# Optimization experiments

Hardware: AMD Instinct MI355X
Metric: run time of the kernel (lower is better)

Reference implementation:

```python
import jax, jax.numpy as jnp
import numpy as np

D_MODEL = 768
N_HEAD = 12
D_K = D_MODEL // N_HEAD
B, S = 2, 2048


def setup_inputs() -> dict:
    key = jax.random.key(0)
    ks = jax.random.split(key, 13)
    scale = 1.0 / np.sqrt(D_MODEL)
    inp = {
        'q': jax.random.normal(ks[0], (B, S, D_MODEL), jnp.float32),
        'k': jax.random.normal(ks[1], (B, S, D_MODEL), jnp.float32),
        'v': jax.random.normal(ks[2], (B, S, D_MODEL), jnp.float32),
        'Wq': jax.random.normal(ks[3], (D_MODEL, D_MODEL), jnp.float32) * scale,
        'bq': jnp.zeros((D_MODEL,), jnp.float32),
        'Wk': jax.random.normal(ks[4], (D_MODEL, D_MODEL), jnp.float32) * scale,
        'bk': jnp.zeros((D_MODEL,), jnp.float32),
        'Wv': jax.random.normal(ks[5], (D_MODEL, D_MODEL), jnp.float32) * scale,
        'bv': jnp.zeros((D_MODEL,), jnp.float32),
        'Wo': jax.random.normal(ks[6], (D_MODEL, D_MODEL), jnp.float32) * scale,
        'bo': jnp.zeros((D_MODEL,), jnp.float32),
        'mask': jax.random.randint(ks[7], (B, 1, S), 0, 2, jnp.int32),
    }
    return inp


def reference(q, k, v, Wq, bq, Wk, bk, Wv, bv, Wo, bo, mask):
    # project and split heads: [B,S,D] -> [B,H,S,Dk]
    def heads(x, W, b):
        y = x @ W + b
        return y.reshape(B, S, N_HEAD, D_K).transpose(0, 2, 1, 3)

    qh = heads(q, Wq, bq)
    kh = heads(k, Wk, bk)
    vh = heads(v, Wv, bv)
    # full score matrix [B,H,S,S] (intentionally materialized, as in source)
    scores = jnp.einsum('bhqd,bhkd->bhqk', qh, kh) / jnp.sqrt(jnp.float32(D_K))
    m = mask[:, None, :, :]  # [B,1,1,S] broadcast over heads and queries
    scores = jnp.where(m == 0, jnp.float32(-1e9), scores)
    p_attn = jax.nn.softmax(scores, axis=-1)
    # dropout omitted (eval / deterministic reference)
    x = jnp.einsum('bhqk,bhkd->bhqd', p_attn, vh)
    x = x.transpose(0, 2, 1, 3).reshape(B, S, D_MODEL)
    return x @ Wo + bo
```

## Files before the change

kernel.cpp:

```cpp
#include <hip/hip_runtime.h>


#define H_ 12
#define DK_ 64
#define B_DIM 2
#define SEQ 2048
#define DM 768
#define MROWS 4096
#define PER_IN ((size_t)MROWS * DM)
#define QSCALE 0.18033688011112042f

typedef short bf16x8 __attribute__((ext_vector_type(8)));
typedef short bf16x4 __attribute__((ext_vector_type(4)));
typedef float f32x4 __attribute__((ext_vector_type(4)));
typedef float f32x16 __attribute__((ext_vector_type(16)));

__device__ inline unsigned short f2bf(float f) {
    union { float f; unsigned int i; } x; x.f = f;
    unsigned int r = x.i + 0x7fff + ((x.i >> 16) & 1);
    return (unsigned short)(r >> 16);
}

__device__ inline unsigned pack2bf(float lo, float hi) {
#if __has_builtin(__builtin_amdgcn_cvt_pk_bf16_f32)
    auto v = __builtin_amdgcn_cvt_pk_bf16_f32(lo, hi);
    return __builtin_bit_cast(unsigned, v);
#else
    return (unsigned)f2bf(lo) | ((unsigned)f2bf(hi) << 16);
#endif
}

__device__ inline float exp2fast(float x) {
#if __has_builtin(__builtin_amdgcn_exp2f)
    return __builtin_amdgcn_exp2f(x);
#else
    return exp2f(x);
#endif
}

__device__ inline f32x16 mfma32x8(bf16x4 a, bf16x4 b, f32x16 c) {
#if __has_builtin(__builtin_amdgcn_mfma_f32_32x32x8bf16_1k)
    return __builtin_amdgcn_mfma_f32_32x32x8bf16_1k(a, b, c, 0, 0, 0);
#else
    asm("v_mfma_f32_32x32x8_bf16 %0, %1, %2, %0" : "+v"(c) : "v"(a), "v"(b));
    return c;
#endif
}

__device__ inline void gload_lds16(const unsigned short* g, unsigned short* ldsbase,
                                   int lane) {
#if __has_builtin(__builtin_amdgcn_global_load_lds)
    __builtin_amdgcn_global_load_lds(
        (const __attribute__((address_space(1))) unsigned int*)g,
        (__attribute__((address_space(3))) unsigned int*)ldsbase, 16, 0, 0);
#else
    *(uint4*)(ldsbase + 8 * lane) = *(const uint4*)g;
#endif
}

__global__ __launch_bounds__(256) void prep(
    const float* __restrict__ q, const float* __restrict__ k,
    const float* __restrict__ v,
    unsigned short* __restrict__ qb, unsigned short* __restrict__ kb,
    unsigned short* __restrict__ vb,
    const float* __restrict__ w0, const float* __restrict__ w1,
    const float* __restrict__ w2, const float* __restrict__ w3,
    unsigned short* __restrict__ wtbase,
    const int* __restrict__ mask, int* __restrict__ idx,
    int* __restrict__ nkeys) {
    __shared__ unsigned short t[32][33];
    __shared__ int wsum[4];
    int job = blockIdx.x, tid = threadIdx.x;
    if (job < 9216) {
        int buf = job / 3072, x = job % 3072;
        const float* src = buf == 0 ? q : (buf == 1 ? k : v);
        unsigned short* dst = buf == 0 ? qb : (buf == 1 ? kb : vb);
        size_t i = ((size_t)x * 256 + tid) * 4;
        float4 f = *(const float4*)(src + i);
        ushort4 u;
        u.x = f2bf(f.x); u.y = f2bf(f.y); u.z = f2bf(f.z); u.w = f2bf(f.w);
        *(ushort4*)(dst + i) = u;
    } else if (job < 11520) {
        int tb = job - 9216;
        int z = tb / 576, r = tb % 576, by = r / 24, bx = r % 24;
        const float* in = z == 0 ? w0 : (z == 1 ? w1 : (z == 2 ? w2 : w3));
        unsigned short* out = wtbase + (size_t)z * DM * DM;
        int x = tid & 31, y = tid >> 5;
        int k0 = bx * 32, n0 = by * 32;
#pragma unroll
        for (int i = 0; i < 32; i += 8)
            t[y + i][x] = f2bf(in[(size_t)(k0 + y + i) * DM + n0 + x]);
        __syncthreads();
#pragma unroll
        for (int i = 0; i < 32; i += 8)
            out[(size_t)(n0 + y + i) * DM + k0 + x] = t[x][y + i];
    } else {
        int b = job - 11520;
        int lane = tid & 63, wave = tid >> 6;
        const int* mp = mask + (size_t)b * SEQ + tid * 8;
        int4 a = *(const int4*)mp;
        int4 c = *(const int4*)(mp + 4);
        int m[8] = {a.x, a.y, a.z, a.w, c.x, c.y, c.z, c.w};
        int pre[8], s = 0;
#pragma unroll
        for (int e = 0; e < 8; e++) { pre[e] = s; s += (m[e] != 0); }
        int incl = s;
#pragma unroll
        for (int off = 1; off < 64; off <<= 1) {
            int vv = __shfl_up(incl, off);
            if (lane >= off) incl += vv;
        }
        int lexcl = incl - s;
        if (lane == 63) wsum[wave] = incl;
        __syncthreads();
        int base = lexcl;
        for (int w = 0; w < wave; w++) base += wsum[w];
#pragma unroll
        for (int e = 0; e < 8; e++)
            if (m[e]) idx[b * SEQ + base + pre[e]] = tid * 8 + e;
        if (tid == 0) nkeys[b] = wsum[0] + wsum[1] + wsum[2] + wsum[3];
    }
}

__global__ __launch_bounds__(256) void gatherKV(const unsigned short* __restrict__ Kh,
                                                const unsigned short* __restrict__ Vn,
                                                const int* __restrict__ idx,
                                                const int* __restrict__ nkeys,
                                                unsigned short* __restrict__ Kc,
                                                unsigned short* __restrict__ Vtc) {
    __shared__ unsigned short Tl[64][72];
    int tid = threadIdx.x;
    int j0 = blockIdx.x * 64, bh = blockIdx.y, b = bh / H_;
    int n = nkeys[b];
    int row = tid >> 2, cb = (tid & 3) * 16;
    int j = j0 + row;
    int src = j < n ? idx[b * SEQ + j] : -1;
    unsigned short v[16];
    unsigned short* ok = Kc + ((size_t)bh * SEQ + j) * DK_ + cb;
    if (src >= 0) {
        const unsigned short* gv = Vn + ((size_t)bh * SEQ + src) * DK_ + cb;
        *(uint4*)&v[0] = *(const uint4*)gv;
        *(uint4*)&v[8] = *(const uint4*)(gv + 8);
        const unsigned short* gk = Kh + ((size_t)bh * SEQ + src) * DK_ + cb;
        uint4 k0 = *(const uint4*)gk;
        uint4 k1 = *(const uint4*)(gk + 8);
        *(uint4*)ok = k0;
        *(uint4*)(ok + 8) = k1;
    } else {
        uint4 z = {0u, 0u, 0u, 0u};
        *(uint4*)&v[0] = z;
        *(uint4*)&v[8] = z;
        *(uint4*)ok = z;
        *(uint4*)(ok + 8) = z;
    }
#pragma unroll
    for (int e = 0; e < 16; e++)
        Tl[cb + e][row] = v[e];
    __syncthreads();
    uint4 o0 = *(const uint4*)&Tl[row][cb];
    uint4 o1 = *(const uint4*)&Tl[row][cb + 8];
    unsigned short* out = Vtc + ((size_t)bh * DK_ + row) * SEQ + j0 + cb;
    *(uint4*)out = o0;
    *(uint4*)(out + 8) = o1;
}

template <int QKV>
__global__ __launch_bounds__(256) void gemm128(
    const unsigned short* __restrict__ A0, const unsigned short* __restrict__ A1,
    const unsigned short* __restrict__ A2, const unsigned short* __restrict__ Wt,
    const float* __restrict__ bias0, const float* __restrict__ bias1,
    const float* __restrict__ bias2,
    void* __restrict__ O0, void* __restrict__ O1, void* __restrict__ O2) {
    __shared__ unsigned short S[2][2][128][64];
    const int K = DM;
    const int NT = K / 64;
    int tid = threadIdx.x;
    int wave = tid >> 6, lane = tid & 63, quad = lane >> 4, l15 = lane & 15;
    int wr = wave >> 1, wc = wave & 1;
    int m0 = blockIdx.x * 128, n0 = blockIdx.y * 128;
    int lrow = lane >> 3, lcol = (lane & 7) * 8;

    int mi = 0, nb0 = n0;
    const unsigned short* A = A0;
    const float* bias = bias0;
    void* O = O0;
    if constexpr (QKV) {
        mi = n0 >= 1536 ? 2 : (n0 >= 768 ? 1 : 0);
        nb0 = n0 - mi * 768;
        A = mi == 0 ? A0 : (mi == 1 ? A1 : A2);
        bias = mi == 0 ? bias0 : (mi == 1 ? bias1 : bias2);
        O = mi == 0 ? O0 : (mi == 1 ? O1 : O2);
    }

    f32x4 acc[4][4];
#pragma unroll
    for (int i = 0; i < 4; i++)
#pragma unroll
        for (int j = 0; j < 4; j++)
#pragma unroll
            for (int r = 0; r < 4; r++) acc[i][j][r] = 0.f;

    const unsigned short* gA = A + (size_t)(m0 + 32 * wave + lrow) * K + lcol;
    const unsigned short* gB = Wt + (size_t)(n0 + 32 * wave + lrow) * K + lcol;

#pragma unroll
    for (int c = 0; c < 4; c++) {
        gload_lds16(gA + (size_t)8 * c * K, &S[0][0][32 * wave + 8 * c][0], lane);
        gload_lds16(gB + (size_t)8 * c * K, &S[0][1][32 * wave + 8 * c][0], lane);
    }

    for (int t = 0; t < NT; t++) {
        int cur = t & 1;
        if (t + 1 < NT) {
            int k0 = (t + 1) * 64;
#pragma unroll
            for (int c = 0; c < 4; c++) {
                gload_lds16(gA + (size_t)8 * c * K + k0, &S[cur ^ 1][0][32 * wave + 8 * c][0], lane);
                gload_lds16(gB + (size_t)8 * c * K + k0, &S[cur ^ 1][1][32 * wave + 8 * c][0], lane);
            }
            asm volatile("s_waitcnt vmcnt(8)" ::: "memory");
        } else {
            asm volatile("s_waitcnt vmcnt(0)" ::: "memory");
        }
        __builtin_amdgcn_s_barrier();

        unsigned short (*Al)[64] = S[cur][0];
        unsigned short (*Bl)[64] = S[cur][1];
#pragma unroll
        for (int ks = 0; ks < 64; ks += 32) {
            bf16x8 af[4], bfr[4];
#pragma unroll
            for (int i = 0; i < 4; i++)
                af[i] = *(const bf16x8*)&Al[64 * wr + 16 * i + l15][ks + 8 * quad];
#pragma unroll
            for (int j = 0; j < 4; j++)
                bfr[j] = *(const bf16x8*)&Bl[64 * wc + 16 * j + l15][ks + 8 * quad];
#pragma unroll
            for (int i = 0; i < 4; i++)
#pragma unroll
                for (int j = 0; j < 4; j++)
                    acc[i][j] = __builtin_amdgcn_mfma_f32_16x16x32_bf16(af[i], bfr[j], acc[i][j], 0, 0, 0);
        }
        asm volatile("" ::: "memory");
        __builtin_amdgcn_s_barrier();
    }

    if constexpr (!QKV) {
#pragma unroll
        for (int j = 0; j < 4; j++) {
            int nn = nb0 + 64 * wc + 16 * j + l15;
            float bv = bias[nn];
#pragma unroll
            for (int i = 0; i < 4; i++)
#pragma unroll
                for (int r = 0; r < 4; r++) {
                    int m = m0 + 64 * wr + 16 * i + 4 * quad + r;
                    ((float*)O0)[(size_t)m * DM + nn] = acc[i][j][r] + bv;
                }
        }
    } else {
        float sc = mi == 0 ? QSCALE : 1.0f;
        __syncthreads();
        unsigned short (*Cl)[128] = (unsigned short(*)[128])S;
#pragma unroll
        for (int j = 0; j < 4; j++) {
            float bv = bias[nb0 + 64 * wc + 16 * j + l15];
#pragma unroll
            for (int i = 0; i < 4; i++)
#pragma unroll
                for (int r = 0; r < 4; r++)
                    Cl[64 * wr + 16 * i + 4 * quad + r][64 * wc + 16 * j + l15] =
                        f2bf((acc[i][j][r] + bv) * sc);
        }
        __syncthreads();
        int row = tid >> 1, half = tid & 1;
        int m = m0 + row;
        int b = m >> 11, s = m & 2047;
        int h = (nb0 + 64 * half) >> 6;
        unsigned short* og = (unsigned short*)O + ((size_t)(b * H_ + h) * SEQ + s) * DK_;
        const unsigned short* cr = &Cl[row][64 * half];
#pragma unroll
        for (int c = 0; c < 4; c++)
            *(uint4*)(og + 16 * c) = *(const uint4*)(cr + 16 * c);
#pragma unroll
        for (int c = 0; c < 4; c++)
            *(uint4*)(og + 16 * c + 8) = *(const uint4*)(cr + 16 * c + 8);
    }
}

__global__ __launch_bounds__(256) void attn_fa(const unsigned short* __restrict__ Q,
                                               const unsigned short* __restrict__ Kc,
                                               const unsigned short* __restrict__ Vtc,
                                               const int* __restrict__ nkeys,
                                               unsigned short* __restrict__ ctx) {
    __shared__ __align__(16) unsigned short Ql[64][72];
    __shared__ __align__(16) unsigned short Kl[64][72];
    __shared__ __align__(16) unsigned short Vl[64][68];
    __shared__ __align__(16) float Op[2][32][32];
    __shared__ __align__(16) float lp[2][32];
    int tid = threadIdx.x;
    int wave = tid >> 6, lane = tid & 63;
    int l31 = lane & 31, hi = lane >> 5;
    int qh = wave & 1, kh = wave >> 1;
    int bh = blockIdx.y, b = bh / H_, h = bh % H_;
    int q0 = blockIdx.x * 64;

    int n = nkeys[b];
    int nt = (n + 63) >> 6;
    float padf = (float)(nt * 64 - n);

    {
        int row = tid >> 2, cb = (tid & 3) * 16;
        const unsigned short* gq = Q + ((size_t)bh * SEQ + q0 + row) * DK_ + cb;
        *(uint4*)&Ql[row][cb]     = *(const uint4*)gq;
        *(uint4*)&Ql[row][cb + 8] = *(const uint4*)(gq + 8);
    }
    __syncthreads();

    bf16x8 qf[4];
#pragma unroll
    for (int c = 0; c < 4; c++)
        qf[c] = *(const bf16x8*)&Ql[32 * qh + l31][16 * c + 8 * hi];

    float lrow = 0.f;
    f32x16 o[2][2];
#pragma unroll
    for (int dt = 0; dt < 2; dt++)
#pragma unroll
        for (int p = 0; p < 2; p++)
#pragma unroll
            for (int r = 0; r < 16; r++) o[dt][p][r] = 0.f;

    int krow = tid >> 2, kcb = (tid & 3) * 16;
    const unsigned short* gk = Kc + ((size_t)bh * SEQ + krow) * DK_ + kcb;
    const unsigned short* gv = Vtc + ((size_t)bh * DK_ + krow) * SEQ + kcb;

    uint4 kr0 = *(const uint4*)gk, kr1 = *(const uint4*)(gk + 8);
    uint4 vr0 = *(const uint4*)gv, vr1 = *(const uint4*)(gv + 8);

    for (int kt = 0; kt < nt; kt++) {
        __syncthreads();
        *(uint4*)&Kl[krow][kcb]     = kr0;
        *(uint4*)&Kl[krow][kcb + 8] = kr1;
        *(uint4*)&Vl[krow][kcb]     = vr0;
        *(uint4*)&Vl[krow][kcb + 8] = vr1;
        __syncthreads();
        if (kt + 1 < nt) {
            gk += (size_t)64 * DK_;
            gv += 64;
            kr0 = *(const uint4*)gk; kr1 = *(const uint4*)(gk + 8);
            vr0 = *(const uint4*)gv; vr1 = *(const uint4*)(gv + 8);
        }

        f32x16 sT;
#pragma unroll
        for (int r = 0; r < 16; r++) sT[r] = 0.f;
#pragma unroll
        for (int c = 0; c < 4; c++) {
            bf16x8 kf = *(const bf16x8*)&Kl[32 * kh + l31][16 * c + 8 * hi];
            sT = __builtin_amdgcn_mfma_f32_32x32x16_bf16(kf, qf[c], sT, 0, 0, 0);
        }

        bf16x4 pfrag[4];
#pragma unroll
        for (int c = 0; c < 4; c++) {
            float p0 = exp2fast(sT[4 * c + 0]);
            float p1 = exp2fast(sT[4 * c + 1]);
            float p2 = exp2fast(sT[4 * c + 2]);
            float p3 = exp2fast(sT[4 * c + 3]);
            lrow += (p0 + p1) + (p2 + p3);
            union { unsigned u[2]; bf16x4 v; } pk;
            pk.u[0] = pack2bf(p0, p1);
            pk.u[1] = pack2bf(p2, p3);
            pfrag[c] = pk.v;
        }

#pragma unroll
        for (int dt = 0; dt < 2; dt++)
#pragma unroll
            for (int c = 0; c < 4; c++) {
                bf16x4 vf = *(const bf16x4*)&Vl[32 * dt + l31][32 * kh + 8 * c + 4 * hi];
                o[dt][c & 1] = mfma32x8(pfrag[c], vf, o[dt][c & 1]);
            }
    }

    lrow += __shfl_xor(lrow, 32);
    float inv = 0.f;
#pragma unroll
    for (int dt = 0; dt < 2; dt++) {
        if (kh == 1) {
#pragma unroll
            for (int r = 0; r < 16; r++) {
                int qrl = (r & 3) + 8 * (r >> 2) + 4 * hi;
                Op[qh][qrl][l31] = o[dt][0][r] + o[dt][1][r];
            }
            if (dt == 0 && hi == 0) lp[qh][l31] = lrow;
        }
        __syncthreads();
        if (kh == 0) {
            if (dt == 0) {
                float l = lrow + lp[qh][l31] - padf;
                inv = l > 0.f ? 1.f / l : 0.f;
            }
#pragma unroll
            for (int r = 0; r < 16; r++) {
                int qrl = (r & 3) + 8 * (r >> 2) + 4 * hi;
                float invr = __shfl(inv, qrl);
                int qg = q0 + 32 * qh + qrl;
                size_t base = ((size_t)b * SEQ + qg) * DM + h * DK_;
                float v = o[dt][0][r] + o[dt][1][r] + Op[qh][qrl][l31];
                ctx[base + 32 * dt + l31] = f2bf(v * invr);
            }
        }
        __syncthreads();
    }
}

extern "C" void kernel_launch(void* const* d_in, const int* in_sizes, int n_in,
                              void* d_out, int out_size, void* d_ws, size_t ws_size,
                              hipStream_t stream) {
    const float* q  = (const float*)d_in[0];
    const float* k  = (const float*)d_in[1];
    const float* v  = (const float*)d_in[2];
    const float* Wq = (const float*)d_in[3];
    const float* bq = (const float*)d_in[4];
    const float* Wk = (const float*)d_in[5];
    const float* bk = (const float*)d_in[6];
    const float* Wv = (const float*)d_in[7];
    const float* bv = (const float*)d_in[8];
    const float* Wo = (const float*)d_in[9];
    const float* bo = (const float*)d_in[10];
    const int* mask = (const int*)d_in[11];

    unsigned short* ws = (unsigned short*)d_ws;
    unsigned short* qb = ws;
    unsigned short* kb = ws + PER_IN;
    unsigned short* vb = ws + 2 * PER_IN;
    unsigned short* Qh = ws + 3 * PER_IN;
    unsigned short* Kh = ws + 4 * PER_IN;
    unsigned short* Vhn = ws + 5 * PER_IN;
    unsigned short* WtQKV = ws + 6 * PER_IN;
    unsigned short* WtO = WtQKV + (size_t)3 * DM * DM;
    unsigned short* Kc = kb;
    unsigned short* Vtc = vb;
    unsigned short* ctx = qb;
    int* idx = (int*)d_out;
    int* nk = idx + B_DIM * SEQ;

    prep<<<dim3(11522), 256, 0, stream>>>(q, k, v, qb, kb, vb,
                                          Wq, Wk, Wv, Wo, WtQKV, mask, idx, nk);

    gemm128<1><<<dim3(MROWS / 128, 3 * DM / 128), 256, 0, stream>>>(
        qb, kb, vb, WtQKV, bq, bk, bv, Qh, Kh, Vhn);

    gatherKV<<<dim3(SEQ / 64, B_DIM * H_), 256, 0, stream>>>(Kh, Vhn, idx, nk, Kc, Vtc);

    attn_fa<<<dim3(SEQ / 64, B_DIM * H_), 256, 0, stream>>>(Qh, Kc, Vtc, nk, ctx);

    gemm128<0><<<dim3(MROWS / 128, DM / 128), 256, 0, stream>>>(
        ctx, ctx, ctx, WtO, bo, bo, bo, d_out, d_out, d_out);
}
```

Measured before the change: 193.0 us.

## Retile output GEMM, swizzle workgroups, compute softmax row sums via MFMA

The GEMM kernel gains an M-tile template parameter. The output projection now uses 64-row tiles, which doubles its workgroup count from 192 to 384 for better CU coverage. Both GEMMs also get an XCD-style workgroup index swizzle meant to improve L2 locality. In attention, the per-lane scalar row-sum accumulation and cross-lane shuffles are replaced by an MFMA against a ones vector, and occupancy is hinted with launch_bounds(256,4). The MFMA sum adds matrix work and accumulator registers while removing VALU adds and shuffles, and the row sums now come from bf16-rounded probabilities.

```diff
diff --git a/kernel.cpp b/kernel.cpp
--- a/kernel.cpp
+++ b/kernel.cpp
@@ -164,20 +164,27 @@
     *(uint4*)(out + 8) = o1;
 }
 
-template <int QKV>
+template <int QKV, int TM>
 __global__ __launch_bounds__(256) void gemm128(
     const unsigned short* __restrict__ A0, const unsigned short* __restrict__ A1,
     const unsigned short* __restrict__ A2, const unsigned short* __restrict__ Wt,
     const float* __restrict__ bias0, const float* __restrict__ bias1,
     const float* __restrict__ bias2,
     void* __restrict__ O0, void* __restrict__ O1, void* __restrict__ O2) {
-    __shared__ unsigned short S[2][2][128][64];
+    __shared__ unsigned short S[2][TM + 128][64];
     const int K = DM;
     const int NT = K / 64;
+    constexpr int NI = TM / 32;
+    constexpr int AC = TM / 32;
     int tid = threadIdx.x;
     int wave = tid >> 6, lane = tid & 63, quad = lane >> 4, l15 = lane & 15;
     int wr = wave >> 1, wc = wave & 1;
-    int m0 = blockIdx.x * 128, n0 = blockIdx.y * 128;
+
+    int nwg = gridDim.x * gridDim.y;
+    int lin = blockIdx.y * gridDim.x + blockIdx.x;
+    int swz = (lin & 7) * (nwg >> 3) + (lin >> 3);
+    int bx = swz % gridDim.x, by = swz / gridDim.x;
+    int m0 = bx * TM, n0 = by * 128;
     int lrow = lane >> 3, lcol = (lane & 7) * 8;
 
     int mi = 0, nb0 = n0;
@@ -192,51 +199,55 @@
         O = mi == 0 ? O0 : (mi == 1 ? O1 : O2);
     }
 
-    f32x4 acc[4][4];
-#pragma unroll
-    for (int i = 0; i < 4; i++)
+    f32x4 acc[NI][4];
+#pragma unroll
+    for (int i = 0; i < NI; i++)
 #pragma unroll
         for (int j = 0; j < 4; j++)
 #pragma unroll
             for (int r = 0; r < 4; r++) acc[i][j][r] = 0.f;
 
-    const unsigned short* gA = A + (size_t)(m0 + 32 * wave + lrow) * K + lcol;
+    const unsigned short* gA = A + (size_t)(m0 + (TM / 4) * wave + lrow) * K + lcol;
     const unsigned short* gB = Wt + (size_t)(n0 + 32 * wave + lrow) * K + lcol;
 
 #pragma unroll
-    for (int c = 0; c < 4; c++) {
-        gload_lds16(gA + (size_t)8 * c * K, &S[0][0][32 * wave + 8 * c][0], lane);
-        gload_lds16(gB + (size_t)8 * c * K, &S[0][1][32 * wave + 8 * c][0], lane);
-    }
+    for (int c = 0; c < AC; c++)
+        gload_lds16(gA + (size_t)8 * c * K, &S[0][(TM / 4) * wave + 8 * c][0], lane);
+#pragma unroll
+    for (int c = 0; c < 4; c++)
+        gload_lds16(gB + (size_t)8 * c * K, &S[0][TM + 32 * wave + 8 * c][0], lane);
 
     for (int t = 0; t < NT; t++) {
         int cur = t & 1;
         if (t + 1 < NT) {
             int k0 = (t + 1) * 64;
 #pragma unroll
-            for (int c = 0; c < 4; c++) {
-                gload_lds16(gA + (size_t)8 * c * K + k0, &S[cur ^ 1][0][32 * wave + 8 * c][0], lane);
-                gload_lds16(gB + (size_t)8 * c * K + k0, &S[cur ^ 1][1][32 * wave + 8 * c][0], lane);
-            }
-            asm volatile("s_waitcnt vmcnt(8)" ::: "memory");
+            for (int c = 0; c < AC; c++)
+                gload_lds16(gA + (size_t)8 * c * K + k0, &S[cur ^ 1][(TM / 4) * wave + 8 * c][0], lane);
+#pragma unroll
+            for (int c = 0; c < 4; c++)
+                gload_lds16(gB + (size_t)8 * c * K + k0, &S[cur ^ 1][TM + 32 * wave + 8 * c][0], lane);
+            if constexpr (TM == 128)
+                asm volatile("s_waitcnt vmcnt(8)" ::: "memory");
+            else
+                asm volatile("s_waitcnt vmcnt(6)" ::: "memory");
         } else {
             asm volatile("s_waitcnt vmcnt(0)" ::: "memory");
         }
         __builtin_amdgcn_s_barrier();
 
-        unsigned short (*Al)[64] = S[cur][0];
-        unsigned short (*Bl)[64] = S[cur][1];
+        unsigned short (*Sl)[64] = S[cur];
 #pragma unroll
         for (int ks = 0; ks < 64; ks += 32) {
-            bf16x8 af[4], bfr[4];
-#pragma unroll
-            for (int i = 0; i < 4; i++)
-                af[i] = *(const bf16x8*)&Al[64 * wr + 16 * i + l15][ks + 8 * quad];
+            bf16x8 af[NI], bfr[4];
+#pragma unroll
+            for (int i = 0; i < NI; i++)
+                af[i] = *(const bf16x8*)&Sl[(TM / 2) * wr + 16 * i + l15][ks + 8 * quad];
 #pragma unroll
             for (int j = 0; j < 4; j++)
-                bfr[j] = *(const bf16x8*)&Bl[64 * wc + 16 * j + l15][ks + 8 * quad];
-#pragma unroll
-            for (int i = 0; i < 4; i++)
+                bfr[j] = *(const bf16x8*)&Sl[TM + 64 * wc + 16 * j + l15][ks + 8 * quad];
+#pragma unroll
+            for (int i = 0; i < NI; i++)
 #pragma unroll
                 for (int j = 0; j < 4; j++)
                     acc[i][j] = __builtin_amdgcn_mfma_f32_16x16x32_bf16(af[i], bfr[j], acc[i][j], 0, 0, 0);
@@ -251,10 +262,10 @@
             int nn = nb0 + 64 * wc + 16 * j + l15;
             float bv = bias[nn];
 #pragma unroll
-            for (int i = 0; i < 4; i++)
+            for (int i = 0; i < NI; i++)
 #pragma unroll
                 for (int r = 0; r < 4; r++) {
-                    int m = m0 + 64 * wr + 16 * i + 4 * quad + r;
+                    int m = m0 + (TM / 2) * wr + 16 * i + 4 * quad + r;
                     ((float*)O0)[(size_t)m * DM + nn] = acc[i][j][r] + bv;
                 }
         }
@@ -266,10 +277,10 @@
         for (int j = 0; j < 4; j++) {
             float bv = bias[nb0 + 64 * wc + 16 * j + l15];
 #pragma unroll
-            for (int i = 0; i < 4; i++)
+            for (int i = 0; i < NI; i++)
 #pragma unroll
                 for (int r = 0; r < 4; r++)
-                    Cl[64 * wr + 16 * i + 4 * quad + r][64 * wc + 16 * j + l15] =
+                    Cl[(TM / 2) * wr + 16 * i + 4 * quad + r][64 * wc + 16 * j + l15] =
                         f2bf((acc[i][j][r] + bv) * sc);
         }
         __syncthreads();
@@ -288,11 +299,11 @@
     }
 }
 
-__global__ __launch_bounds__(256) void attn_fa(const unsigned short* __restrict__ Q,
-                                               const unsigned short* __restrict__ Kc,
-                                               const unsigned short* __restrict__ Vtc,
-                                               const int* __restrict__ nkeys,
-                                               unsigned short* __restrict__ ctx) {
+__global__ __launch_bounds__(256, 4) void attn_fa(const unsigned short* __restrict__ Q,
+                                                  const unsigned short* __restrict__ Kc,
+                                                  const unsigned short* __restrict__ Vtc,
+                                                  const int* __restrict__ nkeys,
+                                                  unsigned short* __restrict__ ctx) {
     __shared__ __align__(16) unsigned short Ql[64][72];
     __shared__ __align__(16) unsigned short Kl[64][72];
     __shared__ __align__(16) unsigned short Vl[64][68];
@@ -322,8 +333,14 @@
     for (int c = 0; c < 4; c++)
         qf[c] = *(const bf16x8*)&Ql[32 * qh + l31][16 * c + 8 * hi];
 
-    float lrow = 0.f;
+    union { unsigned u[2]; bf16x4 v; } onesu;
+    onesu.u[0] = 0x3F803F80u; onesu.u[1] = 0x3F803F80u;
+    bf16x4 ones = onesu.v;
+
     f32x16 o[2][2];
+    f32x16 lsum;
+#pragma unroll
+    for (int r = 0; r < 16; r++) lsum[r] = 0.f;
 #pragma unroll
     for (int dt = 0; dt < 2; dt++)
 #pragma unroll
@@ -368,7 +385,6 @@
             float p1 = exp2fast(sT[4 * c + 1]);
             float p2 = exp2fast(sT[4 * c + 2]);
             float p3 = exp2fast(sT[4 * c + 3]);
-            lrow += (p0 + p1) + (p2 + p3);
             union { unsigned u[2]; bf16x4 v; } pk;
             pk.u[0] = pack2bf(p0, p1);
             pk.u[1] = pack2bf(p2, p3);
@@ -376,6 +392,10 @@
         }
 
 #pragma unroll
+        for (int c = 0; c < 4; c++)
+            lsum = mfma32x8(pfrag[c], ones, lsum);
+
+#pragma unroll
         for (int dt = 0; dt < 2; dt++)
 #pragma unroll
             for (int c = 0; c < 4; c++) {
@@ -384,8 +404,6 @@
             }
     }
 
-    lrow += __shfl_xor(lrow, 32);
-    float inv = 0.f;
 #pragma unroll
     for (int dt = 0; dt < 2; dt++) {
         if (kh == 1) {
@@ -393,23 +411,20 @@
             for (int r = 0; r < 16; r++) {
                 int qrl = (r & 3) + 8 * (r >> 2) + 4 * hi;
                 Op[qh][qrl][l31] = o[dt][0][r] + o[dt][1][r];
+                if (dt == 0 && l31 == 0) lp[qh][qrl] = lsum[r];
             }
-            if (dt == 0 && hi == 0) lp[qh][l31] = lrow;
         }
         __syncthreads();
         if (kh == 0) {
-            if (dt == 0) {
-                float l = lrow + lp[qh][l31] - padf;
-                inv = l > 0.f ? 1.f / l : 0.f;
-            }
 #pragma unroll
             for (int r = 0; r < 16; r++) {
                 int qrl = (r & 3) + 8 * (r >> 2) + 4 * hi;
-                float invr = __shfl(inv, qrl);
+                float l = lsum[r] + lp[qh][qrl] - padf;
+                float iv = l > 0.f ? 1.f / l : 0.f;
                 int qg = q0 + 32 * qh + qrl;
                 size_t base = ((size_t)b * SEQ + qg) * DM + h * DK_;
                 float v = o[dt][0][r] + o[dt][1][r] + Op[qh][qrl][l31];
-                ctx[base + 32 * dt + l31] = f2bf(v * invr);
+                ctx[base + 32 * dt + l31] = f2bf(v * iv);
             }
         }
         __syncthreads();
@@ -450,13 +465,13 @@
     prep<<<dim3(11522), 256, 0, stream>>>(q, k, v, qb, kb, vb,
                                           Wq, Wk, Wv, Wo, WtQKV, mask, idx, nk);
 
-    gemm128<1><<<dim3(MROWS / 128, 3 * DM / 128), 256, 0, stream>>>(
+    gemm128<1, 128><<<dim3(MROWS / 128, 3 * DM / 128), 256, 0, stream>>>(
         qb, kb, vb, WtQKV, bq, bk, bv, Qh, Kh, Vhn);
 
     gatherKV<<<dim3(SEQ / 64, B_DIM * H_), 256, 0, stream>>>(Kh, Vhn, idx, nk, Kc, Vtc);
 
     attn_fa<<<dim3(SEQ / 64, B_DIM * H_), 256, 0, stream>>>(Qh, Kc, Vtc, nk, ctx);
 
-    gemm128<0><<<dim3(MROWS / 128, DM / 128), 256, 0, stream>>>(
+    gemm128<0, 64><<<dim3(MROWS / 64, DM / 128), 256, 0, stream>>>(
         ctx, ctx, ctx, WtO, bo, bo, bo, d_out, d_out, d_out);
 }
```

Result: slower. 221.6 us (+14.9%).
